# Optimization experiments

Hardware: AMD Instinct MI355X
Metric: run time of the kernel (lower is better)

The kernel has to match this reference:

```python
import jax, jax.numpy as jnp
import numpy as np

EMBED_DIM = 1024
NUM_HEADS = 16
HEAD_DIM = EMBED_DIM // NUM_HEADS


def setup_inputs() -> dict:
    key = jax.random.key(0)
    ks = jax.random.split(key, 9)
    B, T, D = 2, 4096, EMBED_DIM
    scale = 1.0 / np.sqrt(D)
    x = jax.random.normal(ks[0], (B, T, D), dtype=jnp.float32)
    # nn.Linear weights stored as (out, in); we use (in, out) layout via transpose-free init
    Wq = jax.random.uniform(ks[1], (D, D), dtype=jnp.float32, minval=-scale, maxval=scale)
    Wk = jax.random.uniform(ks[2], (D, D), dtype=jnp.float32, minval=-scale, maxval=scale)
    Wv = jax.random.uniform(ks[3], (D, D), dtype=jnp.float32, minval=-scale, maxval=scale)
    Wo = jax.random.uniform(ks[4], (D, D), dtype=jnp.float32, minval=-scale, maxval=scale)
    bq = jax.random.uniform(ks[5], (D,), dtype=jnp.float32, minval=-scale, maxval=scale)
    bk = jax.random.uniform(ks[6], (D,), dtype=jnp.float32, minval=-scale, maxval=scale)
    bv = jax.random.uniform(ks[7], (D,), dtype=jnp.float32, minval=-scale, maxval=scale)
    bo = jax.random.uniform(ks[8], (D,), dtype=jnp.float32, minval=-scale, maxval=scale)
    return {"x": x, "Wq": Wq, "bq": bq, "Wk": Wk, "bk": bk,
            "Wv": Wv, "bv": bv, "Wo": Wo, "bo": bo}


def reference(x, Wq, bq, Wk, bk, Wv, bv, Wo, bo):
    B, T, D = x.shape
    H, Hd = NUM_HEADS, HEAD_DIM
    q = x @ Wq + bq  # [B,T,D]
    k = x @ Wk + bk
    v = x @ Wv + bv
    # [B,T,D] -> [B,H,T,Hd]
    q = q.reshape(B, T, H, Hd).transpose(0, 2, 1, 3)
    k = k.reshape(B, T, H, Hd).transpose(0, 2, 1, 3)
    v = v.reshape(B, T, H, Hd).transpose(0, 2, 1, 3)
    att = jnp.einsum('bhqd,bhkd->bhqk', q, k) / jnp.sqrt(jnp.float32(Hd))
    causal = jnp.tril(jnp.ones((T, T), dtype=bool))  # True = keep
    att = jnp.where(causal, att, -jnp.inf)
    att = jax.nn.softmax(att, axis=-1)
    out = jnp.einsum('bhqk,bhkd->bhqd', att, v)  # [B,H,T,Hd]
    out = out.transpose(0, 2, 1, 3).reshape(B, T, D)
    return out @ Wo + bo
```

## Files before the change

kernel.cpp:

```cpp
#include <hip/hip_runtime.h>
#include <hip/hip_bf16.h>
#include <math.h>

typedef __bf16 bf16;
typedef __attribute__((ext_vector_type(8))) __bf16 bf16x8;
typedef __attribute__((ext_vector_type(4))) __bf16 bf16x4;
typedef __attribute__((ext_vector_type(4))) short short4v;
typedef __attribute__((ext_vector_type(4))) float f32x4;

#define MFMA16(a,b,c)  __builtin_amdgcn_mfma_f32_16x16x32_bf16((a),(b),(c),0,0,0)
#define MFMAK16(a,b,c) __builtin_amdgcn_mfma_f32_16x16x16bf16_1k((a),(b),(c),0,0,0)

__device__ __forceinline__ void gload16(const void* gp, void* lp) {
  __builtin_amdgcn_global_load_lds(
      (const __attribute__((address_space(1))) void*)gp,
      (__attribute__((address_space(3))) void*)lp, 16, 0, 0);
}

__global__ __launch_bounds__(256) void cast_x(
    const float* __restrict__ x, bf16* __restrict__ xb)
{
  size_t i = ((size_t)blockIdx.x*256 + threadIdx.x) * 8;
  f32x4 a = *(const f32x4*)(x+i);
  f32x4 b = *(const f32x4*)(x+i+4);
  bf16x8 o;
  #pragma unroll
  for (int j=0;j<4;j++) { o[j] = (bf16)a[j]; o[4+j] = (bf16)b[j]; }
  *(bf16x8*)(xb+i) = o;
}

__global__ __launch_bounds__(1024) void tr_cast(
    const float* __restrict__ w0, const float* __restrict__ w1,
    const float* __restrict__ w2, bf16* __restrict__ dst)
{
  __shared__ bf16 tile[64][65];
  const float* src = (blockIdx.z==0)?w0:(blockIdx.z==1)?w1:w2;
  bf16* d = dst + (size_t)blockIdx.z * (1024*1024);
  int x = threadIdx.x, y = threadIdx.y;
  int tc = blockIdx.x, tr = blockIdx.y;
  #pragma unroll
  for (int i=0;i<4;i++) {
    int r = y + i*16;
    tile[r][x] = (bf16)src[(size_t)(tr*64+r)*1024 + tc*64 + x];
  }
  __syncthreads();
  #pragma unroll
  for (int i=0;i<4;i++) {
    int r = y + i*16;
    d[(size_t)(tc*64+r)*1024 + tr*64 + x] = tile[x][r];
  }
}

__global__ __launch_bounds__(256) void gemm_qkv(
    const bf16* __restrict__ A, const bf16* __restrict__ Bt,
    const float* __restrict__ bq, const float* __restrict__ bk, const float* __restrict__ bv,
    bf16* __restrict__ q, bf16* __restrict__ k, bf16* __restrict__ v,
    int M, int K)
{
  __shared__ __align__(16) bf16 As[128*32];
  __shared__ __align__(16) bf16 Bs[128*32];
  const int tid  = threadIdx.x;
  const int wave = tid >> 6;
  const int lane = tid & 63;
  const int l15  = lane & 15;
  const int quad = lane >> 4;
  const int m0 = blockIdx.y * 128;
  const int n0 = blockIdx.x * 128;
  const int wm = (wave >> 1) * 64;
  const int wn = (wave & 1) * 64;
  const int srow = lane >> 2;
  const int scol = (lane & 3) * 8;

  f32x4 acc[4][4];
  #pragma unroll
  for (int i=0;i<4;i++)
    #pragma unroll
    for (int j=0;j<4;j++)
      acc[i][j] = (f32x4){0.f,0.f,0.f,0.f};

  for (int k0 = 0; k0 < K; k0 += 32) {
    __syncthreads();
    #pragma unroll
    for (int p=0;p<2;p++) {
      int c = p*4 + wave;
      int row = c*16 + srow;
      gload16(A  + (size_t)(m0+row)*K + k0 + scol, As + c*512);
      gload16(Bt + (size_t)(n0+row)*K + k0 + scol, Bs + c*512);
    }
    __syncthreads();
    bf16x8 af[4], bfr[4];
    #pragma unroll
    for (int t=0;t<4;t++) {
      af[t]  = *(const bf16x8*)(As + (wm + t*16 + l15)*32 + quad*8);
      bfr[t] = *(const bf16x8*)(Bs + (wn + t*16 + l15)*32 + quad*8);
    }
    #pragma unroll
    for (int mt=0;mt<4;mt++)
      #pragma unroll
      for (int nt=0;nt<4;nt++)
        acc[mt][nt] = MFMA16(af[mt], bfr[nt], acc[mt][nt]);
  }

  const int mat = n0 >> 10;
  const float* bsel = (mat==0) ? bq : (mat==1) ? bk : bv;
  bf16*       osel  = (mat==0) ? q  : (mat==1) ? k  : v;
  #pragma unroll
  for (int nt=0;nt<4;nt++) {
    int col = n0 + wn + nt*16 + l15;
    int cw  = col & 1023;
    float bvv = bsel[cw];
    #pragma unroll
    for (int mt=0;mt<4;mt++) {
      int row = m0 + wm + mt*16 + quad*4;
      #pragma unroll
      for (int r=0;r<4;r++)
        osel[(size_t)(row + r)*1024 + cw] = (bf16)(acc[mt][nt][r] + bvv);
    }
  }
}

__global__ __launch_bounds__(256) void gemm_out(
    const bf16* __restrict__ A, const bf16* __restrict__ Bt,
    const float* __restrict__ bias, float* __restrict__ C,
    int M, int N, int K)
{
  __shared__ __align__(16) bf16 As[128*32];
  __shared__ __align__(16) bf16 Bs[128*32];
  const int tid  = threadIdx.x;
  const int wave = tid >> 6;
  const int lane = tid & 63;
  const int l15  = lane & 15;
  const int quad = lane >> 4;
  const int m0 = blockIdx.y * 128;
  const int n0 = blockIdx.x * 128;
  const int wm = (wave >> 1) * 64;
  const int wn = (wave & 1) * 64;
  const int srow = lane >> 2;
  const int scol = (lane & 3) * 8;

  f32x4 acc[4][4];
  #pragma unroll
  for (int i=0;i<4;i++)
    #pragma unroll
    for (int j=0;j<4;j++)
      acc[i][j] = (f32x4){0.f,0.f,0.f,0.f};

  for (int k0 = 0; k0 < K; k0 += 32) {
    __syncthreads();
    #pragma unroll
    for (int p=0;p<2;p++) {
      int c = p*4 + wave;
      int row = c*16 + srow;
      gload16(A  + (size_t)(m0+row)*K + k0 + scol, As + c*512);
      gload16(Bt + (size_t)(n0+row)*K + k0 + scol, Bs + c*512);
    }
    __syncthreads();
    bf16x8 af[4], bfr[4];
    #pragma unroll
    for (int t=0;t<4;t++) {
      af[t]  = *(const bf16x8*)(As + (wm + t*16 + l15)*32 + quad*8);
      bfr[t] = *(const bf16x8*)(Bs + (wn + t*16 + l15)*32 + quad*8);
    }
    #pragma unroll
    for (int mt=0;mt<4;mt++)
      #pragma unroll
      for (int nt=0;nt<4;nt++)
        acc[mt][nt] = MFMA16(af[mt], bfr[nt], acc[mt][nt]);
  }

  #pragma unroll
  for (int nt=0;nt<4;nt++) {
    int col = n0 + wn + nt*16 + l15;
    float bvv = bias[col];
    #pragma unroll
    for (int mt=0;mt<4;mt++) {
      int row = m0 + wm + mt*16 + quad*4;
      #pragma unroll
      for (int r=0;r<4;r++)
        C[(size_t)(row + r)*N + col] = acc[mt][nt][r] + bvv;
    }
  }
}

__global__ __launch_bounds__(256, 4) void attn_fwd(
    const bf16* __restrict__ Q, const bf16* __restrict__ Kp,
    const bf16* __restrict__ V, bf16* __restrict__ O)
{
  __shared__ __align__(16) bf16 Ks[2*64*72];
  __shared__ __align__(16) bf16 Vt[2*64*72];

  const int tid  = threadIdx.x;
  const int w    = tid >> 6;
  const int lane = tid & 63;
  const int l15  = lane & 15;
  const int quad = lane >> 4;

  const int bid = blockIdx.x;
  const int qt  = 63 - (bid >> 5);
  const int bh  = bid & 31;
  const int h   = bh & 15;
  const int b   = bh >> 4;

  const size_t headoff = (size_t)h * 64;
  const size_t bbase   = (size_t)b * 4096;

  bf16x8 aq[2];
  {
    int row = qt*64 + w*16 + l15;
    const bf16* qp = Q + (bbase + row)*1024 + headoff + quad*8;
    aq[0] = *(const bf16x8*)(qp);
    aq[1] = *(const bf16x8*)(qp + 32);
  }

  short4v ones_s;
  {
    bf16x4 o1;
    #pragma unroll
    for (int j=0;j<4;j++) o1[j] = (bf16)1.0f;
    ones_s = __builtin_bit_cast(short4v, o1);
  }

  f32x4 acco[4];
  f32x4 accli;
  #pragma unroll
  for (int i=0;i<4;i++) acco[i] = (f32x4){0.f,0.f,0.f,0.f};
  accli = (f32x4){0.f,0.f,0.f,0.f};

  const int kt_row = tid >> 2;
  const int kt_col = (tid & 3) * 16;

  {
    const bf16* kp = Kp + (bbase + kt_row)*1024 + headoff + kt_col;
    bf16x8 k0 = *(const bf16x8*)(kp);
    bf16x8 k1 = *(const bf16x8*)(kp + 8);
    *(bf16x8*)(Ks + kt_row*72 + kt_col)     = k0;
    *(bf16x8*)(Ks + kt_row*72 + kt_col + 8) = k1;
    const bf16* vp = V + (bbase + lane)*1024 + headoff + w*16;
    bf16x8 v0 = *(const bf16x8*)(vp);
    bf16x8 v1 = *(const bf16x8*)(vp + 8);
    #pragma unroll
    for (int j=0;j<8;j++) {
      Vt[(w*16 + j    )*72 + lane] = v0[j];
      Vt[(w*16 + 8 + j)*72 + lane] = v1[j];
    }
  }
  __syncthreads();

  for (int kt = 0; kt <= qt; ++kt) {
    const int p = kt & 1;
    const bool pre = (kt < qt);

    bf16x8 kr0, kr1, vr0, vr1;
    if (pre) {
      const bf16* kp = Kp + (bbase + (size_t)(kt+1)*64 + kt_row)*1024 + headoff + kt_col;
      kr0 = *(const bf16x8*)(kp);
      kr1 = *(const bf16x8*)(kp + 8);
      const bf16* vp = V + (bbase + (size_t)(kt+1)*64 + lane)*1024 + headoff + w*16;
      vr0 = *(const bf16x8*)(vp);
      vr1 = *(const bf16x8*)(vp + 8);
    }

    const bf16* ksb = Ks + p*4608;
    const bf16* vtb = Vt + p*4608;

    f32x4 accs[4];
    #pragma unroll
    for (int i=0;i<4;i++) accs[i] = (f32x4){0.f,0.f,0.f,0.f};
    #pragma unroll
    for (int kk=0;kk<2;kk++) {
      #pragma unroll
      for (int tt=0;tt<4;tt++) {
        bf16x8 ka = *(const bf16x8*)(ksb + (tt*16 + l15)*72 + kk*32 + quad*8);
        accs[tt] = MFMA16(ka, aq[kk], accs[tt]);
      }
    }

    const bool diag = (kt == qt);
    short4v pts[4];
    #pragma unroll
    for (int tt=0;tt<4;tt++) {
      bf16x4 pb;
      #pragma unroll
      for (int r=0;r<4;r++) {
        float tv = fminf(accs[tt][r] * 0.1803368801f, 60.0f);
        float pf = exp2f(tv);
        if (diag && (tt*16 + quad*4 + r > w*16 + l15)) pf = 0.0f;
        pb[r] = (bf16)pf;
      }
      pts[tt] = __builtin_bit_cast(short4v, pb);
    }

    #pragma unroll
    for (int nt=0;nt<4;nt++) {
      #pragma unroll
      for (int tt=0;tt<4;tt++) {
        bf16x4 va = *(const bf16x4*)(vtb + (nt*16 + l15)*72 + tt*16 + quad*4);
        acco[nt] = MFMAK16(__builtin_bit_cast(short4v, va), pts[tt], acco[nt]);
      }
    }
    #pragma unroll
    for (int tt=0;tt<4;tt++)
      accli = MFMAK16(ones_s, pts[tt], accli);

    if (pre) {
      bf16* ksn = Ks + (p^1)*4608;
      bf16* vtn = Vt + (p^1)*4608;
      *(bf16x8*)(ksn + kt_row*72 + kt_col)     = kr0;
      *(bf16x8*)(ksn + kt_row*72 + kt_col + 8) = kr1;
      #pragma unroll
      for (int j=0;j<8;j++) {
        vtn[(w*16 + j    )*72 + lane] = vr0[j];
        vtn[(w*16 + 8 + j)*72 + lane] = vr1[j];
      }
      __syncthreads();
    }
  }

  {
    float inv = 1.0f / accli[0];
    int qrow = qt*64 + w*16 + l15;
    bf16* ob = O + (bbase + qrow)*1024 + headoff;
    #pragma unroll
    for (int nt=0;nt<4;nt++) {
      bf16x4 o;
      #pragma unroll
      for (int r=0;r<4;r++) o[r] = (bf16)(acco[nt][r] * inv);
      *(bf16x4*)(ob + nt*16 + quad*4) = o;
    }
  }
}

extern "C" void kernel_launch(void* const* d_in, const int* in_sizes, int n_in,
                              void* d_out, int out_size, void* d_ws, size_t ws_size,
                              hipStream_t stream) {
  const float* x  = (const float*)d_in[0];
  const float* Wq = (const float*)d_in[1];
  const float* bq = (const float*)d_in[2];
  const float* Wk = (const float*)d_in[3];
  const float* bk = (const float*)d_in[4];
  const float* Wv = (const float*)d_in[5];
  const float* bv = (const float*)d_in[6];
  const float* Wo = (const float*)d_in[7];
  const float* bo = (const float*)d_in[8];
  float* out = (float*)d_out;

  bf16* ws = (bf16*)d_ws;
  bf16* q  = ws;
  bf16* k  = q + (size_t)8192*1024;
  bf16* v  = k + (size_t)8192*1024;
  bf16* xb = v + (size_t)8192*1024;
  bf16* ao = q;
  bf16* WtQKV = (bf16*)d_out;
  bf16* WtO   = xb;

  tr_cast<<<dim3(16,16,3), dim3(64,16), 0, stream>>>(Wq, Wk, Wv, WtQKV);
  cast_x<<<4096, 256, 0, stream>>>(x, xb);
  gemm_qkv<<<dim3(24,64), 256, 0, stream>>>(xb, WtQKV, bq, bk, bv, q, k, v, 8192, 1024);
  tr_cast<<<dim3(16,16,1), dim3(64,16), 0, stream>>>(Wo, Wo, Wo, WtO);
  attn_fwd<<<2048, 256, 0, stream>>>(q, k, v, ao);
  gemm_out<<<dim3(8,64), 256, 0, stream>>>(ao, WtO, bo, out, 8192, 1024, 1024);
}
```

Before: 356.1 us.

## Swizzle attention LDS tiles, fold softmax scale into Q projection, raise occupancy

Replaces the padded K and transposed-V shared-memory tiles with XOR-swizzled unpadded layouts, shrinking LDS per block to allow a launch bound of 5 blocks per CU. The softmax scale (log2e/sqrt(d)) is moved into the Q projection epilogue, removing a multiply per score and using the raw exp2 intrinsic. It also adds s_setprio around the MFMA sections and strength-reduces prefetch address arithmetic. The risk is swizzle index errors and extra register pressure under the tighter occupancy bound.

```diff
diff --git a/kernel.cpp b/kernel.cpp
--- a/kernel.cpp
+++ b/kernel.cpp
@@ -104,6 +104,7 @@
   const int mat = n0 >> 10;
   const float* bsel = (mat==0) ? bq : (mat==1) ? bk : bv;
   bf16*       osel  = (mat==0) ? q  : (mat==1) ? k  : v;
+  const float qsc   = (mat==0) ? 0.1803368801f : 1.0f;
   #pragma unroll
   for (int nt=0;nt<4;nt++) {
     int col = n0 + wn + nt*16 + l15;
@@ -114,7 +115,7 @@
       int row = m0 + wm + mt*16 + quad*4;
       #pragma unroll
       for (int r=0;r<4;r++)
-        osel[(size_t)(row + r)*1024 + cw] = (bf16)(acc[mt][nt][r] + bvv);
+        osel[(size_t)(row + r)*1024 + cw] = (bf16)((acc[mt][nt][r] + bvv) * qsc);
     }
   }
 }
@@ -182,12 +183,12 @@
   }
 }
 
-__global__ __launch_bounds__(256, 4) void attn_fwd(
+__global__ __launch_bounds__(256, 5) void attn_fwd(
     const bf16* __restrict__ Q, const bf16* __restrict__ Kp,
     const bf16* __restrict__ V, bf16* __restrict__ O)
 {
-  __shared__ __align__(16) bf16 Ks[2*64*72];
-  __shared__ __align__(16) bf16 Vt[2*64*72];
+  __shared__ __align__(16) char KsB[2*8192];
+  __shared__ __align__(16) char VtB[2*8192];
 
   const int tid  = threadIdx.x;
   const int w    = tid >> 6;
@@ -227,24 +228,39 @@
   accli = (f32x4){0.f,0.f,0.f,0.f};
 
   const int kt_row = tid >> 2;
-  const int kt_col = (tid & 3) * 16;
+  const int kswz   = (kt_row & 7) << 4;
+  const int ks_w0  = kt_row*128 + (((tid & 3)*32)      ^ kswz);
+  const int ks_w1  = kt_row*128 + (((tid & 3)*32 + 16) ^ kswz);
+  const int vt_wbase = w*2048;
+  const int vt_wlane = 2*lane;
+
+  const int s7    = l15 & 7;
+  const int ks_r0 = l15*128 + ((quad ^ (s7 & 3)) << 4) + ((s7 >> 2) << 6);
+  const int ks_r1 = ks_r0 ^ 64;
+  const int vt_rbase = l15*128 + ((quad ^ (l15 & 3)) << 3) + ((l15 >> 2) << 5);
+  int vt_r[4];
+  #pragma unroll
+  for (int tt=0;tt<4;tt++) vt_r[tt] = vt_rbase ^ (tt << 5);
 
   {
-    const bf16* kp = Kp + (bbase + kt_row)*1024 + headoff + kt_col;
+    const bf16* kp = Kp + (bbase + kt_row)*1024 + headoff + (tid & 3)*16;
     bf16x8 k0 = *(const bf16x8*)(kp);
     bf16x8 k1 = *(const bf16x8*)(kp + 8);
-    *(bf16x8*)(Ks + kt_row*72 + kt_col)     = k0;
-    *(bf16x8*)(Ks + kt_row*72 + kt_col + 8) = k1;
+    *(bf16x8*)(KsB + ks_w0) = k0;
+    *(bf16x8*)(KsB + ks_w1) = k1;
     const bf16* vp = V + (bbase + lane)*1024 + headoff + w*16;
     bf16x8 v0 = *(const bf16x8*)(vp);
     bf16x8 v1 = *(const bf16x8*)(vp + 8);
     #pragma unroll
     for (int j=0;j<8;j++) {
-      Vt[(w*16 + j    )*72 + lane] = v0[j];
-      Vt[(w*16 + 8 + j)*72 + lane] = v1[j];
+      *(bf16*)(VtB + vt_wbase + j*128     + (vt_wlane ^ (j<<3)))     = v0[j];
+      *(bf16*)(VtB + vt_wbase + (8+j)*128 + (vt_wlane ^ ((8+j)<<3))) = v1[j];
     }
   }
   __syncthreads();
+
+  const bf16* kpref = Kp + (bbase + 64 + kt_row)*1024 + headoff + (tid & 3)*16;
+  const bf16* vpref = V  + (bbase + 64 + lane)*1024 + headoff + w*16;
 
   for (int kt = 0; kt <= qt; ++kt) {
     const int p = kt & 1;
@@ -252,28 +268,31 @@
 
     bf16x8 kr0, kr1, vr0, vr1;
     if (pre) {
-      const bf16* kp = Kp + (bbase + (size_t)(kt+1)*64 + kt_row)*1024 + headoff + kt_col;
-      kr0 = *(const bf16x8*)(kp);
-      kr1 = *(const bf16x8*)(kp + 8);
-      const bf16* vp = V + (bbase + (size_t)(kt+1)*64 + lane)*1024 + headoff + w*16;
-      vr0 = *(const bf16x8*)(vp);
-      vr1 = *(const bf16x8*)(vp + 8);
-    }
-
-    const bf16* ksb = Ks + p*4608;
-    const bf16* vtb = Vt + p*4608;
+      kr0 = *(const bf16x8*)(kpref);
+      kr1 = *(const bf16x8*)(kpref + 8);
+      vr0 = *(const bf16x8*)(vpref);
+      vr1 = *(const bf16x8*)(vpref + 8);
+      kpref += 64*1024;
+      vpref += 64*1024;
+    }
+
+    const char* ksb = KsB + p*8192;
+    const char* vtb = VtB + p*8192;
 
     f32x4 accs[4];
     #pragma unroll
     for (int i=0;i<4;i++) accs[i] = (f32x4){0.f,0.f,0.f,0.f};
+
+    __builtin_amdgcn_s_setprio(1);
     #pragma unroll
     for (int kk=0;kk<2;kk++) {
       #pragma unroll
       for (int tt=0;tt<4;tt++) {
-        bf16x8 ka = *(const bf16x8*)(ksb + (tt*16 + l15)*72 + kk*32 + quad*8);
+        bf16x8 ka = *(const bf16x8*)(ksb + (kk ? ks_r1 : ks_r0) + tt*2048);
         accs[tt] = MFMA16(ka, aq[kk], accs[tt]);
       }
     }
+    __builtin_amdgcn_s_setprio(0);
 
     const bool diag = (kt == qt);
     short4v pts[4];
@@ -282,35 +301,37 @@
       bf16x4 pb;
       #pragma unroll
       for (int r=0;r<4;r++) {
-        float tv = fminf(accs[tt][r] * 0.1803368801f, 60.0f);
-        float pf = exp2f(tv);
+        float tv = fminf(accs[tt][r], 60.0f);
+        float pf = __builtin_amdgcn_exp2f(tv);
         if (diag && (tt*16 + quad*4 + r > w*16 + l15)) pf = 0.0f;
         pb[r] = (bf16)pf;
       }
       pts[tt] = __builtin_bit_cast(short4v, pb);
     }
 
+    __builtin_amdgcn_s_setprio(1);
     #pragma unroll
     for (int nt=0;nt<4;nt++) {
       #pragma unroll
       for (int tt=0;tt<4;tt++) {
-        bf16x4 va = *(const bf16x4*)(vtb + (nt*16 + l15)*72 + tt*16 + quad*4);
+        bf16x4 va = *(const bf16x4*)(vtb + vt_r[tt] + nt*2048);
         acco[nt] = MFMAK16(__builtin_bit_cast(short4v, va), pts[tt], acco[nt]);
       }
     }
     #pragma unroll
     for (int tt=0;tt<4;tt++)
       accli = MFMAK16(ones_s, pts[tt], accli);
+    __builtin_amdgcn_s_setprio(0);
 
     if (pre) {
-      bf16* ksn = Ks + (p^1)*4608;
-      bf16* vtn = Vt + (p^1)*4608;
-      *(bf16x8*)(ksn + kt_row*72 + kt_col)     = kr0;
-      *(bf16x8*)(ksn + kt_row*72 + kt_col + 8) = kr1;
+      char* ksn = KsB + (p^1)*8192;
+      char* vtn = VtB + (p^1)*8192;
+      *(bf16x8*)(ksn + ks_w0) = kr0;
+      *(bf16x8*)(ksn + ks_w1) = kr1;
       #pragma unroll
       for (int j=0;j<8;j++) {
-        vtn[(w*16 + j    )*72 + lane] = vr0[j];
-        vtn[(w*16 + 8 + j)*72 + lane] = vr1[j];
+        *(bf16*)(vtn + vt_wbase + j*128     + (vt_wlane ^ (j<<3)))     = vr0[j];
+        *(bf16*)(vtn + vt_wbase + (8+j)*128 + (vt_wlane ^ ((8+j)<<3))) = vr1[j];
       }
       __syncthreads();
     }
```

After: 340.8 us. 4.3% less time.
